# Performance work log

Hardware: AMD Instinct MI355X
Metric: run time of the kernel (lower is better)

The kernel has to match this reference:

```python
import jax, jax.numpy as jnp
import numpy as np

N_QUBITS = 16
DIM = 2 ** N_QUBITS


def _rot_gate(angles):
    """Build combined single-qubit gate Rz @ Ry @ Rx from 3 real angles."""
    rx_a, ry_a, rz_a = angles[0], angles[1], angles[2]
    cx = jnp.cos(rx_a / 2).astype(jnp.complex64)
    sx = jnp.sin(rx_a / 2).astype(jnp.complex64)
    rx = jnp.stack([jnp.stack([cx, -1j * sx]), jnp.stack([-1j * sx, cx])])
    cy = jnp.cos(ry_a / 2).astype(jnp.complex64)
    sy = jnp.sin(ry_a / 2).astype(jnp.complex64)
    ry = jnp.stack([jnp.stack([cy, -sy]), jnp.stack([sy, cy])])
    ez = jnp.exp(-1j * rz_a.astype(jnp.complex64) / 2)
    zero = jnp.zeros((), jnp.complex64)
    rz = jnp.stack([jnp.stack([ez, zero]), jnp.stack([zero, jnp.conj(ez)])])
    return rz @ ry @ rx  # [2, 2] complex64


def _evolve(gates):
    """Apply per-qubit 2x2 gates to |0...0> via butterfly reshapes.

    Qubit q is the q-th least-significant bit (matches torch bit indexing),
    so its axis has stride 2**q: state -> [2**(n-1-q), 2, 2**q].
    """
    state = jnp.zeros(DIM, jnp.complex64).at[0].set(1.0)
    for q in range(N_QUBITS):
        st = state.reshape(2 ** (N_QUBITS - 1 - q), 2, 2 ** q)
        st = jnp.einsum('ab,hbl->hal', gates[q], st)
        state = st.reshape(DIM)
    return jnp.abs(state) ** 2  # probabilities, real float32


def reference(input_embedding, rotation_angles):
    # angles[b, q, :] = embedding_slice + learned offsets (rotation branch)
    B = input_embedding.shape[0]
    angles = input_embedding[:, : N_QUBITS * 3].reshape(B, N_QUBITS, 3) + rotation_angles
    gates = jax.vmap(jax.vmap(_rot_gate))(angles)  # [B, Q, 2, 2]
    return jax.vmap(_evolve)(gates)  # [B, DIM]


def setup_inputs() -> dict:
    key = jax.random.key(0)
    k1, k2 = jax.random.split(key)
    input_embedding = jax.random.normal(k1, (256, 768), dtype=jnp.float32)
    rotation_angles = jax.random.normal(k2, (N_QUBITS, 3), dtype=jnp.float32) * 0.1
    return {"input_embedding": input_embedding, "rotation_angles": rotation_angles}
```

## Files before the change

### kernel.cpp

```cpp
#include <hip/hip_runtime.h>

#define NQ 16
#define DIM 65536
#define BPB 8
#define CHUNK (DIM / BPB)

typedef float f32x4 __attribute__((ext_vector_type(4)));

__global__ __launch_bounds__(256) void qprob_kernel(
    const float* __restrict__ emb,
    const float* __restrict__ rot,
    float* __restrict__ out)
{
    __shared__ float p0s[NQ], p1s[NQ];
    __shared__ float low8[256];
    __shared__ float high8[256];

    const int b = blockIdx.x / BPB;
    const int j = blockIdx.x % BPB;
    const int t = threadIdx.x;

    if (t < NQ) {
        const float rx = emb[b * 768 + t * 3 + 0] + rot[t * 3 + 0];
        const float ry = emb[b * 768 + t * 3 + 1] + rot[t * 3 + 1];
        float sx, cx, sy, cy;
        sincosf(rx * 0.5f, &sx, &cx);
        sincosf(ry * 0.5f, &sy, &cy);
        const float cx2 = cx * cx, sx2 = sx * sx;
        const float cy2 = cy * cy, sy2 = sy * sy;
        p0s[t] = cx2 * cy2 + sx2 * sy2;
        p1s[t] = cx2 * sy2 + sx2 * cy2;
    }
    __syncthreads();

    float lo = 1.0f, hi = 1.0f;
#pragma unroll
    for (int q = 0; q < 8; ++q) {
        lo *= ((t >> q) & 1) ? p1s[q]     : p0s[q];
        hi *= ((t >> q) & 1) ? p1s[q + 8] : p0s[q + 8];
    }
    low8[t] = lo;
    high8[t] = hi;
    __syncthreads();

    const int l = (4 * t) & 255;
    const f32x4 lv = *(const f32x4*)&low8[l];

    const int hb = j * (CHUNK >> 8) + (t >> 6);
    float h[CHUNK / 1024];
#pragma unroll
    for (int k = 0; k < CHUNK / 1024; ++k)
        h[k] = high8[hb + 4 * k];

    f32x4* outrow = (f32x4*)(out + (size_t)b * DIM + (size_t)j * CHUNK);
#pragma unroll
    for (int k = 0; k < CHUNK / 1024; ++k) {
        const f32x4 v = lv * h[k];
        __builtin_nontemporal_store(v, &outrow[k * 256 + t]);
    }
}

extern "C" void kernel_launch(void* const* d_in, const int* in_sizes, int n_in,
                              void* d_out, int out_size, void* d_ws, size_t ws_size,
                              hipStream_t stream) {
    const float* emb = (const float*)d_in[0];
    const float* rot = (const float*)d_in[1];
    float* out = (float*)d_out;

    const int B = in_sizes[0] / 768;
    dim3 grid(B * BPB), block(256);
    qprob_kernel<<<grid, block, 0, stream>>>(emb, rot, out);
}
```

Measured before the change: 16.66 us.

## Split into table-building kernel and pure write kernel via workspace

Adds a small kernel that computes the per-batch low/high 8-qubit probability tables once (instead of redundantly in each of the 8 blocks per batch) and stores them to workspace. A second kernel reads the tables and streams the output with nontemporal stores, with no sincos or syncthreads. The cost is an extra launch and a global round trip through workspace. The original fused kernel stays as a fallback when the workspace is too small.

```diff
diff --git a/kernel.cpp b/kernel.cpp
--- a/kernel.cpp
+++ b/kernel.cpp
@@ -4,8 +4,72 @@
 #define DIM 65536
 #define BPB 8
 #define CHUNK (DIM / BPB)
+#define TAB_BYTES (256 * 512 * 4)
 
 typedef float f32x4 __attribute__((ext_vector_type(4)));
+
+
+__global__ __launch_bounds__(64) void qtab_kernel(
+    const float* __restrict__ emb,
+    const float* __restrict__ rot,
+    float* __restrict__ ws)
+{
+    __shared__ float p0s[NQ], p1s[NQ];
+    const int b = blockIdx.x;
+    const int t = threadIdx.x;
+
+    if (t < NQ) {
+        const float rx = emb[b * 768 + t * 3 + 0] + rot[t * 3 + 0];
+        const float ry = emb[b * 768 + t * 3 + 1] + rot[t * 3 + 1];
+        float sx, cx, sy, cy;
+        sincosf(rx * 0.5f, &sx, &cx);
+        sincosf(ry * 0.5f, &sy, &cy);
+        const float cx2 = cx * cx, sx2 = sx * sx;
+        const float cy2 = cy * cy, sy2 = sy * sy;
+        p0s[t] = cx2 * cy2 + sx2 * sy2;
+        p1s[t] = cx2 * sy2 + sx2 * cy2;
+    }
+    __syncthreads();
+
+    f32x4 lo4, hi4;
+#pragma unroll
+    for (int e = 0; e < 4; ++e) {
+        const int idx = t * 4 + e;
+        float lo = 1.0f, hi = 1.0f;
+#pragma unroll
+        for (int q = 0; q < 8; ++q) {
+            lo *= ((idx >> q) & 1) ? p1s[q]     : p0s[q];
+            hi *= ((idx >> q) & 1) ? p1s[q + 8] : p0s[q + 8];
+        }
+        lo4[e] = lo;
+        hi4[e] = hi;
+    }
+    *(f32x4*)&ws[b * 512 + t * 4]       = lo4;
+    *(f32x4*)&ws[b * 512 + 256 + t * 4] = hi4;
+}
+
+__global__ __launch_bounds__(256) void qwrite_kernel(
+    const float* __restrict__ ws,
+    float* __restrict__ out)
+{
+    const int b = blockIdx.x / BPB;
+    const int j = blockIdx.x % BPB;
+    const int t = threadIdx.x;
+    const float* tab = ws + b * 512;
+
+    const f32x4 lv = *(const f32x4*)&tab[(4 * t) & 255];
+
+    const int hb = j * (CHUNK >> 8) + (t >> 6);
+    float h[CHUNK / 1024];
+#pragma unroll
+    for (int k = 0; k < CHUNK / 1024; ++k)
+        h[k] = tab[256 + hb + 4 * k];
+
+    f32x4* outrow = (f32x4*)(out + (size_t)b * DIM + (size_t)j * CHUNK);
+#pragma unroll
+    for (int k = 0; k < CHUNK / 1024; ++k)
+        __builtin_nontemporal_store(lv * h[k], &outrow[k * 256 + t]);
+}
 
 __global__ __launch_bounds__(256) void qprob_kernel(
     const float* __restrict__ emb,
@@ -54,10 +118,8 @@
 
     f32x4* outrow = (f32x4*)(out + (size_t)b * DIM + (size_t)j * CHUNK);
 #pragma unroll
-    for (int k = 0; k < CHUNK / 1024; ++k) {
-        const f32x4 v = lv * h[k];
-        __builtin_nontemporal_store(v, &outrow[k * 256 + t]);
-    }
+    for (int k = 0; k < CHUNK / 1024; ++k)
+        __builtin_nontemporal_store(lv * h[k], &outrow[k * 256 + t]);
 }
 
 extern "C" void kernel_launch(void* const* d_in, const int* in_sizes, int n_in,
@@ -68,6 +130,12 @@
     float* out = (float*)d_out;
 
     const int B = in_sizes[0] / 768;
-    dim3 grid(B * BPB), block(256);
-    qprob_kernel<<<grid, block, 0, stream>>>(emb, rot, out);
+
+    if (ws_size >= (size_t)TAB_BYTES) {
+        float* ws = (float*)d_ws;
+        qtab_kernel<<<dim3(B), dim3(64), 0, stream>>>(emb, rot, ws);
+        qwrite_kernel<<<dim3(B * BPB), dim3(256), 0, stream>>>(ws, out);
+    } else {
+        qprob_kernel<<<dim3(B * BPB), dim3(256), 0, stream>>>(emb, rot, out);
+    }
 }
```

After: 20.93 us. 1.26x slower.
